# Performance work log

Measured on AMD Instinct MI355X. Metric: run time of the kernel, lower is better.

Reference implementation:

```python
import jax, jax.numpy as jnp
import numpy as np

N_NODES = 500000
N_EDGES = 5000000
D = 16


def _glorot(key, shape):
    fan_in, fan_out = shape[1], shape[0]
    lim = (6.0 / (fan_in + fan_out)) ** 0.5
    return jax.random.uniform(key, shape, jnp.float32, -lim, lim)


def setup_inputs() -> dict:
    key = jax.random.key(0)
    ks = jax.random.split(key, 12)
    x = jax.random.normal(ks[0], (N_NODES, D), jnp.float32)
    edge_index = jax.random.randint(ks[1], (2, N_EDGES), 0, N_NODES, jnp.int32)
    # GraphConv params: lin_rel (weight+bias, applied to aggregated neighbors),
    # lin_root (weight only, applied to self features)
    conv1_w_rel = _glorot(ks[2], (D, D))
    conv1_b_rel = jnp.zeros((D,), jnp.float32)
    conv1_w_root = _glorot(ks[3], (D, D))
    conv2_w_rel = _glorot(ks[4], (D, D))
    conv2_b_rel = jnp.zeros((D,), jnp.float32)
    conv2_w_root = _glorot(ks[5], (D, D))
    fc1_w = _glorot(ks[6], (8, D))
    fc1_b = jnp.zeros((8,), jnp.float32)
    fc2_w = _glorot(ks[7], (2, 8))
    fc2_b = jnp.zeros((2,), jnp.float32)
    return {
        "x": x, "edge_index": edge_index,
        "conv1_w_rel": conv1_w_rel, "conv1_b_rel": conv1_b_rel, "conv1_w_root": conv1_w_root,
        "conv2_w_rel": conv2_w_rel, "conv2_b_rel": conv2_b_rel, "conv2_w_root": conv2_w_root,
        "fc1_w": fc1_w, "fc1_b": fc1_b, "fc2_w": fc2_w, "fc2_b": fc2_b,
    }


def graph_conv(x, edge_index, w_rel, b_rel, w_root):
    # PyG GraphConv (aggr='add'): out_i = W_rel @ sum_{j->i} x_j + b_rel + W_root @ x_i
    src, dst = edge_index[0], edge_index[1]
    msgs = x[src]  # [E, D] gather of source-node features
    agg = jax.ops.segment_sum(msgs, dst, num_segments=x.shape[0])  # [N, D]
    return agg @ w_rel.T + b_rel + x @ w_root.T


def reference(x, edge_index,
              conv1_w_rel, conv1_b_rel, conv1_w_root,
              conv2_w_rel, conv2_b_rel, conv2_w_root,
              fc1_w, fc1_b, fc2_w, fc2_b):
    h = jax.nn.relu(graph_conv(x, edge_index, conv1_w_rel, conv1_b_rel, conv1_w_root))
    h = jax.nn.relu(graph_conv(h, edge_index, conv2_w_rel, conv2_b_rel, conv2_w_root))
    h = jax.nn.relu(h @ fc1_w.T + fc1_b)
    return h @ fc2_w.T + fc2_b
```

## Files before the change

kernel.cpp:

```cpp
#include <hip/hip_runtime.h>

#define N_NODES 500000
#define N_EDGES 5000000
#define D 16

__global__ __launch_bounds__(256) void scatter_add_kernel(
    const float* __restrict__ feat,
    const int* __restrict__ edge_index,
    float* __restrict__ agg) {
    long tid = (long)blockIdx.x * blockDim.x + threadIdx.x;
    long total = (long)N_EDGES * D;
    if (tid >= total) return;
    int e = (int)(tid >> 4);
    int d = (int)(tid & 15);
    int s = edge_index[e];
    int t = edge_index[N_EDGES + e];
    float v = feat[(long)s * D + d];
    atomicAdd(&agg[(long)t * D + d], v);
}

__global__ __launch_bounds__(256) void node1_kernel(
    const float* __restrict__ x,
    const float* __restrict__ agg,
    const float* __restrict__ w_rel,
    const float* __restrict__ b_rel,
    const float* __restrict__ w_root,
    float* __restrict__ h) {
    __shared__ float sWrel[D * D];
    __shared__ float sWroot[D * D];
    __shared__ float sB[D];
    for (int i = threadIdx.x; i < D * D; i += blockDim.x) {
        sWrel[i] = w_rel[i];
        sWroot[i] = w_root[i];
    }
    if (threadIdx.x < D) sB[threadIdx.x] = b_rel[threadIdx.x];
    __syncthreads();

    int i = blockIdx.x * blockDim.x + threadIdx.x;
    if (i >= N_NODES) return;

    float a[D], xi[D];
    {
        const float4* ap = (const float4*)(agg + (long)i * D);
        const float4* xp = (const float4*)(x + (long)i * D);
        #pragma unroll
        for (int q = 0; q < 4; ++q) {
            float4 av = ap[q];
            float4 xv = xp[q];
            a[q * 4 + 0] = av.x; a[q * 4 + 1] = av.y; a[q * 4 + 2] = av.z; a[q * 4 + 3] = av.w;
            xi[q * 4 + 0] = xv.x; xi[q * 4 + 1] = xv.y; xi[q * 4 + 2] = xv.z; xi[q * 4 + 3] = xv.w;
        }
    }

    float4* hp = (float4*)(h + (long)i * D);
    #pragma unroll
    for (int q = 0; q < 4; ++q) {
        float4 o;
        float* op = &o.x;
        #pragma unroll
        for (int r = 0; r < 4; ++r) {
            int dd = q * 4 + r;
            float acc = sB[dd];
            #pragma unroll
            for (int k = 0; k < D; ++k)
                acc += a[k] * sWrel[dd * D + k] + xi[k] * sWroot[dd * D + k];
            op[r] = acc > 0.f ? acc : 0.f;
        }
        hp[q] = o;
    }
}

__global__ __launch_bounds__(256) void node2_kernel(
    const float* __restrict__ h1,
    const float* __restrict__ agg,
    const float* __restrict__ w_rel,
    const float* __restrict__ b_rel,
    const float* __restrict__ w_root,
    const float* __restrict__ fc1_w,
    const float* __restrict__ fc1_b,
    const float* __restrict__ fc2_w,
    const float* __restrict__ fc2_b,
    float* __restrict__ out) {
    __shared__ float sWrel[D * D];
    __shared__ float sWroot[D * D];
    __shared__ float sB[D];
    __shared__ float sF1w[8 * D];
    __shared__ float sF1b[8];
    __shared__ float sF2w[2 * 8];
    __shared__ float sF2b[2];
    for (int i = threadIdx.x; i < D * D; i += blockDim.x) {
        sWrel[i] = w_rel[i];
        sWroot[i] = w_root[i];
    }
    if (threadIdx.x < D) sB[threadIdx.x] = b_rel[threadIdx.x];
    if (threadIdx.x < 8 * D) sF1w[threadIdx.x] = fc1_w[threadIdx.x];
    if (threadIdx.x < 8) sF1b[threadIdx.x] = fc1_b[threadIdx.x];
    if (threadIdx.x < 16) sF2w[threadIdx.x] = fc2_w[threadIdx.x];
    if (threadIdx.x < 2) sF2b[threadIdx.x] = fc2_b[threadIdx.x];
    __syncthreads();

    int i = blockIdx.x * blockDim.x + threadIdx.x;
    if (i >= N_NODES) return;

    float a[D], xi[D];
    {
        const float4* ap = (const float4*)(agg + (long)i * D);
        const float4* xp = (const float4*)(h1 + (long)i * D);
        #pragma unroll
        for (int q = 0; q < 4; ++q) {
            float4 av = ap[q];
            float4 xv = xp[q];
            a[q * 4 + 0] = av.x; a[q * 4 + 1] = av.y; a[q * 4 + 2] = av.z; a[q * 4 + 3] = av.w;
            xi[q * 4 + 0] = xv.x; xi[q * 4 + 1] = xv.y; xi[q * 4 + 2] = xv.z; xi[q * 4 + 3] = xv.w;
        }
    }

    float h2[D];
    #pragma unroll
    for (int dd = 0; dd < D; ++dd) {
        float acc = sB[dd];
        #pragma unroll
        for (int k = 0; k < D; ++k)
            acc += a[k] * sWrel[dd * D + k] + xi[k] * sWroot[dd * D + k];
        h2[dd] = acc > 0.f ? acc : 0.f;
    }

    float h3[8];
    #pragma unroll
    for (int j = 0; j < 8; ++j) {
        float acc = sF1b[j];
        #pragma unroll
        for (int k = 0; k < D; ++k) acc += h2[k] * sF1w[j * D + k];
        h3[j] = acc > 0.f ? acc : 0.f;
    }

    float2 o;
    {
        float acc0 = sF2b[0], acc1 = sF2b[1];
        #pragma unroll
        for (int j = 0; j < 8; ++j) {
            acc0 += h3[j] * sF2w[0 * 8 + j];
            acc1 += h3[j] * sF2w[1 * 8 + j];
        }
        o.x = acc0;
        o.y = acc1;
    }
    ((float2*)out)[i] = o;
}

extern "C" void kernel_launch(void* const* d_in, const int* in_sizes, int n_in,
                              void* d_out, int out_size, void* d_ws, size_t ws_size,
                              hipStream_t stream) {
    const float* x          = (const float*)d_in[0];
    const int*   edge_index = (const int*)d_in[1];
    const float* c1_wrel    = (const float*)d_in[2];
    const float* c1_brel    = (const float*)d_in[3];
    const float* c1_wroot   = (const float*)d_in[4];
    const float* c2_wrel    = (const float*)d_in[5];
    const float* c2_brel    = (const float*)d_in[6];
    const float* c2_wroot   = (const float*)d_in[7];
    const float* fc1_w      = (const float*)d_in[8];
    const float* fc1_b      = (const float*)d_in[9];
    const float* fc2_w      = (const float*)d_in[10];
    const float* fc2_b      = (const float*)d_in[11];
    float* out = (float*)d_out;

    float* agg = (float*)d_ws;
    float* h1  = agg + (long)N_NODES * D;
    size_t feat_bytes = (size_t)N_NODES * D * sizeof(float);

    const int BLK = 256;
    long scatter_total = (long)N_EDGES * D;
    int scatter_blocks = (int)((scatter_total + BLK - 1) / BLK);
    int node_blocks = (N_NODES + BLK - 1) / BLK;

    hipMemsetAsync(agg, 0, feat_bytes, stream);
    scatter_add_kernel<<<scatter_blocks, BLK, 0, stream>>>(x, edge_index, agg);
    node1_kernel<<<node_blocks, BLK, 0, stream>>>(x, agg, c1_wrel, c1_brel, c1_wroot, h1);

    hipMemsetAsync(agg, 0, feat_bytes, stream);
    scatter_add_kernel<<<scatter_blocks, BLK, 0, stream>>>(h1, edge_index, agg);
    node2_kernel<<<node_blocks, BLK, 0, stream>>>(h1, agg, c2_wrel, c2_brel, c2_wroot,
                                                  fc1_w, fc1_b, fc2_w, fc2_b, out);
}
```

Measured before the change: 702.6 us.

## Bin edges by destination bucket and aggregate in LDS with fp16 features

Replaces the global-atomic edge scatter with a counting-sort pass that bins edges into 512-node destination buckets and packs source and local destination into one word. Each layer kernel then accumulates its bucket in shared memory with LDS atomics and applies the dense transforms in the same block, fusing scatter and node updates. Node features and the hidden layer are stored in fp16 to halve gather traffic. This adds histogram, scan and binning kernels, and the fp16 storage reduces precision.

```diff
diff --git a/kernel.cpp b/kernel.cpp
--- a/kernel.cpp
+++ b/kernel.cpp
@@ -1,151 +1,282 @@
 #include <hip/hip_runtime.h>
+#include <hip/hip_fp16.h>
 
 #define N_NODES 500000
 #define N_EDGES 5000000
 #define D 16
 
-__global__ __launch_bounds__(256) void scatter_add_kernel(
-    const float* __restrict__ feat,
-    const int* __restrict__ edge_index,
-    float* __restrict__ agg) {
-    long tid = (long)blockIdx.x * blockDim.x + threadIdx.x;
-    long total = (long)N_EDGES * D;
-    if (tid >= total) return;
-    int e = (int)(tid >> 4);
-    int d = (int)(tid & 15);
-    int s = edge_index[e];
-    int t = edge_index[N_EDGES + e];
-    float v = feat[(long)s * D + d];
-    atomicAdd(&agg[(long)t * D + d], v);
-}
-
-__global__ __launch_bounds__(256) void node1_kernel(
-    const float* __restrict__ x,
-    const float* __restrict__ agg,
-    const float* __restrict__ w_rel,
-    const float* __restrict__ b_rel,
+#define BSH 9
+#define BN (1 << BSH)
+#define NB ((N_NODES + BN - 1) >> BSH)
+#define SRC_BITS 19
+#define SRC_MASK ((1u << SRC_BITS) - 1)
+#define BIN_CHUNK 8192
+#define NBIN_BLOCKS ((N_EDGES + BIN_CHUNK - 1) / BIN_CHUNK)
+
+__global__ __launch_bounds__(256) void cast_kernel(
+    const float* __restrict__ x, __half2* __restrict__ x16) {
+    int i = blockIdx.x * 256 + threadIdx.x;
+    if (i < N_NODES * 8) {
+        float2 v = ((const float2*)x)[i];
+        x16[i] = __float22half2_rn(v);
+    }
+}
+
+__global__ __launch_bounds__(256) void hist_kernel(
+    const int* __restrict__ edge_index, int* __restrict__ cnt) {
+    __shared__ int h[NB];
+    for (int i = threadIdx.x; i < NB; i += 256) h[i] = 0;
+    __syncthreads();
+    int stride = gridDim.x * 256;
+    for (int e = blockIdx.x * 256 + threadIdx.x; e < N_EDGES; e += stride)
+        atomicAdd(&h[edge_index[N_EDGES + e] >> BSH], 1);
+    __syncthreads();
+    for (int i = threadIdx.x; i < NB; i += 256)
+        if (h[i]) atomicAdd(&cnt[i], h[i]);
+}
+
+__global__ __launch_bounds__(256) void scan_kernel(
+    const int* __restrict__ cnt, int* __restrict__ base, int* __restrict__ cursor) {
+    __shared__ int sums[256];
+    int t = threadIdx.x;
+    int v[4]; int ts = 0;
+    #pragma unroll
+    for (int j = 0; j < 4; ++j) {
+        int i = t * 4 + j;
+        v[j] = (i < NB) ? cnt[i] : 0;
+        ts += v[j];
+    }
+    sums[t] = ts;
+    __syncthreads();
+    for (int off = 1; off < 256; off <<= 1) {
+        int val = (t >= off) ? sums[t - off] : 0;
+        __syncthreads();
+        if (t >= off) sums[t] += val;
+        __syncthreads();
+    }
+    int p = sums[t] - ts;
+    #pragma unroll
+    for (int j = 0; j < 4; ++j) {
+        int i = t * 4 + j;
+        if (i < NB) { base[i] = p; cursor[i] = p; }
+        p += v[j];
+    }
+    if (t == 255) base[NB] = p;
+}
+
+__global__ __launch_bounds__(256) void bin_kernel(
+    const int* __restrict__ edge_index, int* __restrict__ cursor,
+    unsigned int* __restrict__ binned) {
+    __shared__ unsigned int buf[BIN_CHUNK];
+    __shared__ unsigned short bufB[BIN_CHUNK];
+    __shared__ int hist[NB];
+    __shared__ int lofs[NB];
+    __shared__ int gofs[NB];
+    __shared__ int sums[256];
+
+    int t = threadIdx.x;
+    int start = blockIdx.x * BIN_CHUNK;
+    int count = min(BIN_CHUNK, N_EDGES - start);
+
+    for (int i = t; i < NB; i += 256) hist[i] = 0;
+    __syncthreads();
+    for (int k = t; k < count; k += 256)
+        atomicAdd(&hist[edge_index[N_EDGES + start + k] >> BSH], 1);
+    __syncthreads();
+
+    int v[4]; int ts = 0;
+    #pragma unroll
+    for (int j = 0; j < 4; ++j) {
+        int i = t * 4 + j;
+        v[j] = (i < NB) ? hist[i] : 0;
+        ts += v[j];
+    }
+    sums[t] = ts;
+    __syncthreads();
+    for (int off = 1; off < 256; off <<= 1) {
+        int val = (t >= off) ? sums[t - off] : 0;
+        __syncthreads();
+        if (t >= off) sums[t] += val;
+        __syncthreads();
+    }
+    int p = sums[t] - ts;
+    #pragma unroll
+    for (int j = 0; j < 4; ++j) {
+        int i = t * 4 + j;
+        if (i < NB) lofs[i] = p;
+        p += v[j];
+    }
+    __syncthreads();
+
+    for (int i = t; i < NB; i += 256) {
+        int c = hist[i];
+        gofs[i] = c ? atomicAdd(&cursor[i], c) : 0;
+    }
+    __syncthreads();
+    for (int i = t; i < NB; i += 256) hist[i] = lofs[i];
+    __syncthreads();
+
+    for (int k = t; k < count; k += 256) {
+        int s = edge_index[start + k];
+        int d = edge_index[N_EDGES + start + k];
+        int b = d >> BSH;
+        int pos = atomicAdd(&hist[b], 1);
+        buf[pos] = (unsigned int)s | ((unsigned int)(d & (BN - 1)) << SRC_BITS);
+        bufB[pos] = (unsigned short)b;
+    }
+    __syncthreads();
+
+    for (int i = t; i < count; i += 256) {
+        int b = bufB[i];
+        binned[gofs[b] + (i - lofs[b])] = buf[i];
+    }
+}
+
+__global__ __launch_bounds__(512) void layer1_kernel(
+    const __half* __restrict__ x16,
+    const unsigned int* __restrict__ binned,
+    const int* __restrict__ base,
+    const float* __restrict__ w_rel, const float* __restrict__ b_rel,
     const float* __restrict__ w_root,
-    float* __restrict__ h) {
-    __shared__ float sWrel[D * D];
-    __shared__ float sWroot[D * D];
-    __shared__ float sB[D];
-    for (int i = threadIdx.x; i < D * D; i += blockDim.x) {
-        sWrel[i] = w_rel[i];
-        sWroot[i] = w_root[i];
-    }
-    if (threadIdx.x < D) sB[threadIdx.x] = b_rel[threadIdx.x];
-    __syncthreads();
-
-    int i = blockIdx.x * blockDim.x + threadIdx.x;
-    if (i >= N_NODES) return;
-
-    float a[D], xi[D];
-    {
-        const float4* ap = (const float4*)(agg + (long)i * D);
-        const float4* xp = (const float4*)(x + (long)i * D);
-        #pragma unroll
-        for (int q = 0; q < 4; ++q) {
-            float4 av = ap[q];
-            float4 xv = xp[q];
-            a[q * 4 + 0] = av.x; a[q * 4 + 1] = av.y; a[q * 4 + 2] = av.z; a[q * 4 + 3] = av.w;
-            xi[q * 4 + 0] = xv.x; xi[q * 4 + 1] = xv.y; xi[q * 4 + 2] = xv.z; xi[q * 4 + 3] = xv.w;
+    __half* __restrict__ h1out) {
+    __shared__ float agg[BN * D];
+    __shared__ float sWrelT[D * D], sWrootT[D * D], sB[D];
+    int t = threadIdx.x;
+    if (t < 256) {
+        int r = t >> 4, c = t & 15;
+        sWrelT[c * D + r] = w_rel[r * D + c];
+        sWrootT[c * D + r] = w_root[r * D + c];
+        if (t < D) sB[t] = b_rel[t];
+    }
+    for (int i = t; i < BN * D; i += 512) agg[i] = 0.f;
+    __syncthreads();
+
+    int bkt = blockIdx.x;
+    int e0 = base[bkt], e1 = base[bkt + 1];
+    int q = t & 3;
+    #pragma unroll 2
+    for (int idx = e0 + (t >> 2); idx < e1; idx += 128) {
+        unsigned int entry = binned[idx];
+        int src = entry & SRC_MASK;
+        int dl = entry >> SRC_BITS;
+        float2 raw = ((const float2*)(x16 + (long)src * D))[q];
+        float2 fa = __half22float2(((__half2*)&raw)[0]);
+        float2 fb = __half22float2(((__half2*)&raw)[1]);
+        float* ap = &agg[dl * D + q * 4];
+        atomicAdd(ap + 0, fa.x);
+        atomicAdd(ap + 1, fa.y);
+        atomicAdd(ap + 2, fb.x);
+        atomicAdd(ap + 3, fb.y);
+    }
+    __syncthreads();
+
+    int d = t & 15;
+    for (int n = (t >> 4); n < BN; n += 32) {
+        int node = (bkt << BSH) + n;
+        if (node >= N_NODES) continue;
+        const float2* xr = (const float2*)(x16 + (long)node * D);
+        float xk[D];
+        #pragma unroll
+        for (int qq = 0; qq < 4; ++qq) {
+            float2 raw = xr[qq];
+            float2 fa = __half22float2(((__half2*)&raw)[0]);
+            float2 fb = __half22float2(((__half2*)&raw)[1]);
+            xk[qq * 4 + 0] = fa.x; xk[qq * 4 + 1] = fa.y;
+            xk[qq * 4 + 2] = fb.x; xk[qq * 4 + 3] = fb.y;
         }
-    }
-
-    float4* hp = (float4*)(h + (long)i * D);
-    #pragma unroll
-    for (int q = 0; q < 4; ++q) {
-        float4 o;
-        float* op = &o.x;
-        #pragma unroll
-        for (int r = 0; r < 4; ++r) {
-            int dd = q * 4 + r;
-            float acc = sB[dd];
+        float acc = sB[d];
+        #pragma unroll
+        for (int k = 0; k < D; ++k)
+            acc += agg[n * D + k] * sWrelT[k * D + d] + xk[k] * sWrootT[k * D + d];
+        h1out[(long)node * D + d] = __float2half(acc > 0.f ? acc : 0.f);
+    }
+}
+
+__global__ __launch_bounds__(512) void layer2_kernel(
+    const __half* __restrict__ h1,
+    const unsigned int* __restrict__ binned,
+    const int* __restrict__ base,
+    const float* __restrict__ w_rel, const float* __restrict__ b_rel,
+    const float* __restrict__ w_root,
+    const float* __restrict__ fc1_w, const float* __restrict__ fc1_b,
+    const float* __restrict__ fc2_w, const float* __restrict__ fc2_b,
+    float* __restrict__ out) {
+    __shared__ float agg[BN * D];
+    __shared__ float sWrelT[D * D], sWrootT[D * D], sB[D];
+    __shared__ float sF1w[8 * D], sF1b[8], sF2w[2 * 8], sF2b[2];
+    int t = threadIdx.x;
+    if (t < 256) {
+        int r = t >> 4, c = t & 15;
+        sWrelT[c * D + r] = w_rel[r * D + c];
+        sWrootT[c * D + r] = w_root[r * D + c];
+        if (t < D) sB[t] = b_rel[t];
+        if (t < 8 * D) sF1w[t] = fc1_w[t];
+        if (t < 8) sF1b[t] = fc1_b[t];
+        if (t < 16) sF2w[t] = fc2_w[t];
+        if (t < 2) sF2b[t] = fc2_b[t];
+    }
+    for (int i = t; i < BN * D; i += 512) agg[i] = 0.f;
+    __syncthreads();
+
+    int bkt = blockIdx.x;
+    int e0 = base[bkt], e1 = base[bkt + 1];
+    int q = t & 3;
+    #pragma unroll 2
+    for (int idx = e0 + (t >> 2); idx < e1; idx += 128) {
+        unsigned int entry = binned[idx];
+        int src = entry & SRC_MASK;
+        int dl = entry >> SRC_BITS;
+        float2 raw = ((const float2*)(h1 + (long)src * D))[q];
+        float2 fa = __half22float2(((__half2*)&raw)[0]);
+        float2 fb = __half22float2(((__half2*)&raw)[1]);
+        float* ap = &agg[dl * D + q * 4];
+        atomicAdd(ap + 0, fa.x);
+        atomicAdd(ap + 1, fa.y);
+        atomicAdd(ap + 2, fb.x);
+        atomicAdd(ap + 3, fb.y);
+    }
+    __syncthreads();
+
+    int d = t & 15;
+    for (int n = (t >> 4); n < BN; n += 32) {
+        int node = (bkt << BSH) + n;
+        if (node >= N_NODES) continue;
+        const float2* xr = (const float2*)(h1 + (long)node * D);
+        float xk[D];
+        #pragma unroll
+        for (int qq = 0; qq < 4; ++qq) {
+            float2 raw = xr[qq];
+            float2 fa = __half22float2(((__half2*)&raw)[0]);
+            float2 fb = __half22float2(((__half2*)&raw)[1]);
+            xk[qq * 4 + 0] = fa.x; xk[qq * 4 + 1] = fa.y;
+            xk[qq * 4 + 2] = fb.x; xk[qq * 4 + 3] = fb.y;
+        }
+        float acc = sB[d];
+        #pragma unroll
+        for (int k = 0; k < D; ++k)
+            acc += agg[n * D + k] * sWrelT[k * D + d] + xk[k] * sWrootT[k * D + d];
+        agg[n * D + d] = acc > 0.f ? acc : 0.f;
+    }
+    __syncthreads();
+
+    for (int it = 0; it < 2; ++it) {
+        int task = t + it * 512;
+        int n = task >> 1, dd = task & 1;
+        int node = (bkt << BSH) + n;
+        if (node >= N_NODES) continue;
+        float h3[8];
+        #pragma unroll
+        for (int j = 0; j < 8; ++j) {
+            float acc = sF1b[j];
             #pragma unroll
-            for (int k = 0; k < D; ++k)
-                acc += a[k] * sWrel[dd * D + k] + xi[k] * sWroot[dd * D + k];
-            op[r] = acc > 0.f ? acc : 0.f;
+            for (int k = 0; k < D; ++k) acc += agg[n * D + k] * sF1w[j * D + k];
+            h3[j] = acc > 0.f ? acc : 0.f;
         }
-        hp[q] = o;
-    }
-}
-
-__global__ __launch_bounds__(256) void node2_kernel(
-    const float* __restrict__ h1,
-    const float* __restrict__ agg,
-    const float* __restrict__ w_rel,
-    const float* __restrict__ b_rel,
-    const float* __restrict__ w_root,
-    const float* __restrict__ fc1_w,
-    const float* __restrict__ fc1_b,
-    const float* __restrict__ fc2_w,
-    const float* __restrict__ fc2_b,
-    float* __restrict__ out) {
-    __shared__ float sWrel[D * D];
-    __shared__ float sWroot[D * D];
-    __shared__ float sB[D];
-    __shared__ float sF1w[8 * D];
-    __shared__ float sF1b[8];
-    __shared__ float sF2w[2 * 8];
-    __shared__ float sF2b[2];
-    for (int i = threadIdx.x; i < D * D; i += blockDim.x) {
-        sWrel[i] = w_rel[i];
-        sWroot[i] = w_root[i];
-    }
-    if (threadIdx.x < D) sB[threadIdx.x] = b_rel[threadIdx.x];
-    if (threadIdx.x < 8 * D) sF1w[threadIdx.x] = fc1_w[threadIdx.x];
-    if (threadIdx.x < 8) sF1b[threadIdx.x] = fc1_b[threadIdx.x];
-    if (threadIdx.x < 16) sF2w[threadIdx.x] = fc2_w[threadIdx.x];
-    if (threadIdx.x < 2) sF2b[threadIdx.x] = fc2_b[threadIdx.x];
-    __syncthreads();
-
-    int i = blockIdx.x * blockDim.x + threadIdx.x;
-    if (i >= N_NODES) return;
-
-    float a[D], xi[D];
-    {
-        const float4* ap = (const float4*)(agg + (long)i * D);
-        const float4* xp = (const float4*)(h1 + (long)i * D);
-        #pragma unroll
-        for (int q = 0; q < 4; ++q) {
-            float4 av = ap[q];
-            float4 xv = xp[q];
-            a[q * 4 + 0] = av.x; a[q * 4 + 1] = av.y; a[q * 4 + 2] = av.z; a[q * 4 + 3] = av.w;
-            xi[q * 4 + 0] = xv.x; xi[q * 4 + 1] = xv.y; xi[q * 4 + 2] = xv.z; xi[q * 4 + 3] = xv.w;
-        }
-    }
-
-    float h2[D];
-    #pragma unroll
-    for (int dd = 0; dd < D; ++dd) {
-        float acc = sB[dd];
-        #pragma unroll
-        for (int k = 0; k < D; ++k)
-            acc += a[k] * sWrel[dd * D + k] + xi[k] * sWroot[dd * D + k];
-        h2[dd] = acc > 0.f ? acc : 0.f;
-    }
-
-    float h3[8];
-    #pragma unroll
-    for (int j = 0; j < 8; ++j) {
-        float acc = sF1b[j];
-        #pragma unroll
-        for (int k = 0; k < D; ++k) acc += h2[k] * sF1w[j * D + k];
-        h3[j] = acc > 0.f ? acc : 0.f;
-    }
-
-    float2 o;
-    {
-        float acc0 = sF2b[0], acc1 = sF2b[1];
-        #pragma unroll
-        for (int j = 0; j < 8; ++j) {
-            acc0 += h3[j] * sF2w[0 * 8 + j];
-            acc1 += h3[j] * sF2w[1 * 8 + j];
-        }
-        o.x = acc0;
-        o.y = acc1;
-    }
-    ((float2*)out)[i] = o;
+        float o = sF2b[dd];
+        #pragma unroll
+        for (int j = 0; j < 8; ++j) o += h3[j] * sF2w[dd * 8 + j];
+        out[(long)node * 2 + dd] = o;
+    }
 }
 
 extern "C" void kernel_launch(void* const* d_in, const int* in_sizes, int n_in,
@@ -165,21 +296,23 @@
     const float* fc2_b      = (const float*)d_in[11];
     float* out = (float*)d_out;
 
-    float* agg = (float*)d_ws;
-    float* h1  = agg + (long)N_NODES * D;
-    size_t feat_bytes = (size_t)N_NODES * D * sizeof(float);
-
-    const int BLK = 256;
-    long scatter_total = (long)N_EDGES * D;
-    int scatter_blocks = (int)((scatter_total + BLK - 1) / BLK);
-    int node_blocks = (N_NODES + BLK - 1) / BLK;
-
-    hipMemsetAsync(agg, 0, feat_bytes, stream);
-    scatter_add_kernel<<<scatter_blocks, BLK, 0, stream>>>(x, edge_index, agg);
-    node1_kernel<<<node_blocks, BLK, 0, stream>>>(x, agg, c1_wrel, c1_brel, c1_wroot, h1);
-
-    hipMemsetAsync(agg, 0, feat_bytes, stream);
-    scatter_add_kernel<<<scatter_blocks, BLK, 0, stream>>>(h1, edge_index, agg);
-    node2_kernel<<<node_blocks, BLK, 0, stream>>>(h1, agg, c2_wrel, c2_brel, c2_wroot,
-                                                  fc1_w, fc1_b, fc2_w, fc2_b, out);
-}
+    __half2* x16h2 = (__half2*)d_ws;
+    __half*  x16   = (__half*)d_ws;
+    __half*  h1    = (__half*)((char*)d_ws + (size_t)N_NODES * D * 2);
+    unsigned int* binned = (unsigned int*)((char*)d_ws + 2 * (size_t)N_NODES * D * 2);
+    int* cnt    = (int*)(binned + N_EDGES);
+    int* base   = cnt + NB;
+    int* cursor = base + (NB + 1);
+
+    hipMemsetAsync(cnt, 0, NB * sizeof(int), stream);
+    cast_kernel<<<(N_NODES * 8 + 255) / 256, 256, 0, stream>>>(x, x16h2);
+    hist_kernel<<<1024, 256, 0, stream>>>(edge_index, cnt);
+    scan_kernel<<<1, 256, 0, stream>>>(cnt, base, cursor);
+    bin_kernel<<<NBIN_BLOCKS, 256, 0, stream>>>(edge_index, cursor, binned);
+
+    layer1_kernel<<<NB, 512, 0, stream>>>(
+        x16, binned, base, c1_wrel, c1_brel, c1_wroot, h1);
+    layer2_kernel<<<NB, 512, 0, stream>>>(
+        h1, binned, base, c2_wrel, c2_brel, c2_wroot,
+        fc1_w, fc1_b, fc2_w, fc2_b, out);
+}
```

New measurement: 1.132 ms. 61.1% more time.
